# Performance work log

Measured on AMD Instinct MI355X. Metric: run time of the kernel, lower is better.

The kernel has to match this reference:

```python
import jax, jax.numpy as jnp
import numpy as np

T, H, O = 32768, 1024, 1024

def setup_inputs() -> dict:
    key = jax.random.key(0)
    k0, k1, k2 = jax.random.split(key, 3)
    dec_h = jax.random.normal(k0, (1, O), dtype=jnp.float32)
    enc = jax.random.normal(k1, (T, 1, H), dtype=jnp.float32)
    attn_w = jax.random.normal(k2, (1, O + H), dtype=jnp.float32) * 0.02
    attn_b = jnp.zeros((1,), dtype=jnp.float32)
    return {"dec_h": dec_h, "enc": enc, "attn_w": attn_w, "attn_b": attn_b}

def reference(dec_h, enc, attn_w, attn_b):
    # dec_h: [1, O]; enc: [T, 1, H]; attn_w: [1, O+H] (cat order: dec then enc)
    t, _, h = enc.shape
    o = dec_h.shape[1]
    enc2d = enc.reshape(t, h)                     # [T, H]
    w_dec = attn_w[:, :o]                         # [1, O]
    w_enc = attn_w[:, o:]                         # [1, H]
    # per-timestep Bahdanau score, vectorized over T
    scores = enc2d @ w_enc.T + (dec_h @ w_dec.T + attn_b)  # [T,1] + [1,1] -> [T,1]
    normalized_weights = jax.nn.softmax(scores.reshape(1, t), axis=1)  # [1, T]
    output = normalized_weights @ enc2d           # [1, H]
    return output, normalized_weights
```

## Files before the change

### kernel.cpp

```cpp
#include <hip/hip_runtime.h>
#include <hip/hip_bf16.h>

constexpr int T = 32768;
constexpr int H = 1024;
constexpr int NB = 512;
constexpr int RPB = T / NB;

constexpr int SC_OFF = 64;
constexpr int PART_OFF = SC_OFF + T;

__global__ void scores_kernel(const float* __restrict__ enc,
                              const float* __restrict__ w_enc,
                              float* __restrict__ scores) {
    const int gwave = (blockIdx.x * blockDim.x + threadIdx.x) >> 6;
    const int lane  = threadIdx.x & 63;
    if (gwave >= T) return;
    const float4* rowp = reinterpret_cast<const float4*>(enc + (size_t)gwave * H);
    const float4* wp   = reinterpret_cast<const float4*>(w_enc);
    float acc = 0.f;
#pragma unroll
    for (int p = 0; p < H / (64 * 4); ++p) {
        float4 e = rowp[lane + p * 64];
        float4 w = wp[lane + p * 64];
        acc += e.x * w.x + e.y * w.y + e.z * w.z + e.w * w.w;
    }
#pragma unroll
    for (int off = 32; off; off >>= 1) acc += __shfl_down(acc, off);
    if (lane == 0) scores[gwave] = acc;
}

__global__ void reduce_ml(const float* __restrict__ sc,
                          float* __restrict__ ml,
                          float* __restrict__ outvec) {
    __shared__ float sm[16];
    const int tid = threadIdx.x;
    if (tid < H) outvec[tid] = 0.f;

    float m = -1e30f;
    for (int t = tid; t < T; t += 1024) m = fmaxf(m, sc[t]);
#pragma unroll
    for (int off = 32; off; off >>= 1) m = fmaxf(m, __shfl_down(m, off));
    if ((tid & 63) == 0) sm[tid >> 6] = m;
    __syncthreads();
    if (tid < 16) {
        float v = sm[tid];
#pragma unroll
        for (int off = 8; off; off >>= 1) v = fmaxf(v, __shfl_down(v, off));
        if (tid == 0) sm[0] = v;
    }
    __syncthreads();
    const float M = sm[0];
    __syncthreads();

    float l = 0.f;
    for (int t = tid; t < T; t += 1024) l += expf(sc[t] - M);
#pragma unroll
    for (int off = 32; off; off >>= 1) l += __shfl_down(l, off);
    if ((tid & 63) == 0) sm[tid >> 6] = l;
    __syncthreads();
    if (tid == 0) {
        float L = 0.f;
#pragma unroll
        for (int i = 0; i < 16; ++i) L += sm[i];
        ml[0] = M;
        ml[1] = L;
    }
}

__global__ void weighted_kernel(const float* __restrict__ enc,
                                const float* __restrict__ sc,
                                const float* __restrict__ ml,
                                float* __restrict__ wout,
                                float* __restrict__ partials) {
    const int b = blockIdx.x;
    const int tid = threadIdx.x;
    const float M = ml[0];
    const float rL = 1.f / ml[1];
    const int row0 = b * RPB;

    if (tid < RPB) wout[row0 + tid] = expf(sc[row0 + tid] - M) * rL;

    float4 acc = make_float4(0.f, 0.f, 0.f, 0.f);
#pragma unroll 4
    for (int r = 0; r < RPB; ++r) {
        const size_t row = (size_t)(row0 + r);
        const float w = expf(sc[row] - M) * rL;
        float4 e = *reinterpret_cast<const float4*>(enc + row * H + (size_t)tid * 4);
        acc.x = fmaf(w, e.x, acc.x);
        acc.y = fmaf(w, e.y, acc.y);
        acc.z = fmaf(w, e.z, acc.z);
        acc.w = fmaf(w, e.w, acc.w);
    }
    *reinterpret_cast<float4*>(partials + (size_t)b * H + (size_t)tid * 4) = acc;
}

__global__ void finalize_kernel(const float* __restrict__ partials,
                                float* __restrict__ out) {
    const int h = blockIdx.x * blockDim.x + threadIdx.x;
    float s = 0.f;
#pragma unroll 8
    for (int b = 0; b < NB; ++b) s += partials[(size_t)b * H + h];
    out[h] = s;
}

extern "C" void kernel_launch(void* const* d_in, const int* in_sizes, int n_in,
                              void* d_out, int out_size, void* d_ws, size_t ws_size,
                              hipStream_t stream) {
    const float* enc    = (const float*)d_in[1];
    const float* attn_w = (const float*)d_in[2];
    const float* w_enc  = attn_w + 1024;

    float* out  = (float*)d_out;
    float* wout = (float*)d_out + H;

    float* ws       = (float*)d_ws;
    float* ml       = ws;
    float* scores   = ws + SC_OFF;
    float* partials = ws + PART_OFF;

    scores_kernel<<<T / 4, 256, 0, stream>>>(enc, w_enc, scores);
    reduce_ml<<<1, 1024, 0, stream>>>(scores, ml, out);
    weighted_kernel<<<NB, 256, 0, stream>>>(enc, scores, ml, wout, partials);
    finalize_kernel<<<H / 256, 256, 0, stream>>>(partials, out);
}
```

Measured before the change: 249.3 us.

## Fuse score, online softmax and weighted sum into a single pass over enc

```diff
diff --git a/kernel.cpp b/kernel.cpp
--- a/kernel.cpp
+++ b/kernel.cpp
@@ -3,104 +3,161 @@
 
 constexpr int T = 32768;
 constexpr int H = 1024;
-constexpr int NB = 512;
-constexpr int RPB = T / NB;
 
-constexpr int SC_OFF = 64;
-constexpr int PART_OFF = SC_OFF + T;
+constexpr int NB1 = 1024;
+constexpr int RPB = T / NB1;
+constexpr int CH  = 8;
 
-__global__ void scores_kernel(const float* __restrict__ enc,
-                              const float* __restrict__ w_enc,
-                              float* __restrict__ scores) {
-    const int gwave = (blockIdx.x * blockDim.x + threadIdx.x) >> 6;
-    const int lane  = threadIdx.x & 63;
-    if (gwave >= T) return;
-    const float4* rowp = reinterpret_cast<const float4*>(enc + (size_t)gwave * H);
-    const float4* wp   = reinterpret_cast<const float4*>(w_enc);
-    float acc = 0.f;
+constexpr int ML_OFF  = 0;
+constexpr int MB_OFF  = 256;
+constexpr int LB_OFF  = MB_OFF + NB1;
+constexpr int SC_OFF  = 4096;
+constexpr int ACC_OFF = SC_OFF + T;
+
+__global__ __launch_bounds__(256) void fused_pass1(
+    const float* __restrict__ enc, const float* __restrict__ w_enc,
+    float* __restrict__ scores, float* __restrict__ mb, float* __restrict__ lb,
+    float* __restrict__ accs) {
+    const int b    = blockIdx.x;
+    const int tid  = threadIdx.x;
+    const int wave = tid >> 6;
+    const int lane = tid & 63;
+    const int row0 = b * RPB;
+
+    const float4 w4 = *reinterpret_cast<const float4*>(w_enc + 4 * tid);
+
+    __shared__ float red[4][CH];
+
+    float  m = -1e30f, l = 0.f;
+    float4 acc = make_float4(0.f, 0.f, 0.f, 0.f);
+
+    for (int c = 0; c < RPB / CH; ++c) {
+        const int r0 = row0 + c * CH;
+        float4 e[CH];
+        float  p[CH];
 #pragma unroll
-    for (int p = 0; p < H / (64 * 4); ++p) {
-        float4 e = rowp[lane + p * 64];
-        float4 w = wp[lane + p * 64];
-        acc += e.x * w.x + e.y * w.y + e.z * w.z + e.w * w.w;
+        for (int r = 0; r < CH; ++r) {
+            e[r] = *reinterpret_cast<const float4*>(enc + (size_t)(r0 + r) * H + 4 * tid);
+            p[r] = e[r].x * w4.x + e[r].y * w4.y + e[r].z * w4.z + e[r].w * w4.w;
+        }
+#pragma unroll
+        for (int r = 0; r < CH; ++r) {
+#pragma unroll
+            for (int off = 32; off; off >>= 1) p[r] += __shfl_xor(p[r], off);
+        }
+        if (lane == 0) {
+#pragma unroll
+            for (int r = 0; r < CH; ++r) red[wave][r] = p[r];
+        }
+        __syncthreads();
+        float s[CH];
+        float mc = -1e30f;
+#pragma unroll
+        for (int r = 0; r < CH; ++r) {
+            s[r] = red[0][r] + red[1][r] + red[2][r] + red[3][r];
+            mc = fmaxf(mc, s[r]);
+        }
+        __syncthreads();
+
+        const float mn  = fmaxf(m, mc);
+        const float rs  = __expf(m - mn);
+        l *= rs;
+        acc.x *= rs; acc.y *= rs; acc.z *= rs; acc.w *= rs;
+#pragma unroll
+        for (int r = 0; r < CH; ++r) {
+            const float wgt = __expf(s[r] - mn);
+            l += wgt;
+            acc.x = fmaf(wgt, e[r].x, acc.x);
+            acc.y = fmaf(wgt, e[r].y, acc.y);
+            acc.z = fmaf(wgt, e[r].z, acc.z);
+            acc.w = fmaf(wgt, e[r].w, acc.w);
+        }
+        m = mn;
+
+        if (tid == 0) {
+#pragma unroll
+            for (int r = 0; r < CH; ++r) scores[r0 + r] = s[r];
+        }
     }
-#pragma unroll
-    for (int off = 32; off; off >>= 1) acc += __shfl_down(acc, off);
-    if (lane == 0) scores[gwave] = acc;
+
+    *reinterpret_cast<float4*>(accs + (size_t)b * H + 4 * tid) = acc;
+    if (tid == 0) { mb[b] = m; lb[b] = l; }
 }
 
-__global__ void reduce_ml(const float* __restrict__ sc,
-                          float* __restrict__ ml,
-                          float* __restrict__ outvec) {
+__global__ __launch_bounds__(1024) void reduce2(
+    const float* __restrict__ mb, const float* __restrict__ lb,
+    float* __restrict__ ml, float* __restrict__ out) {
     __shared__ float sm[16];
-    const int tid = threadIdx.x;
-    if (tid < H) outvec[tid] = 0.f;
+    const int tid  = threadIdx.x;
+    const int wave = tid >> 6;
+    const int lane = tid & 63;
 
-    float m = -1e30f;
-    for (int t = tid; t < T; t += 1024) m = fmaxf(m, sc[t]);
+    out[tid] = 0.f;
+
+    const float mv = mb[tid];
+    float m = mv;
 #pragma unroll
-    for (int off = 32; off; off >>= 1) m = fmaxf(m, __shfl_down(m, off));
-    if ((tid & 63) == 0) sm[tid >> 6] = m;
+    for (int off = 32; off; off >>= 1) m = fmaxf(m, __shfl_xor(m, off));
+    if (lane == 0) sm[wave] = m;
     __syncthreads();
-    if (tid < 16) {
-        float v = sm[tid];
+    if (tid < 64) {
+        float v = (lane < 16) ? sm[lane] : -1e30f;
 #pragma unroll
-        for (int off = 8; off; off >>= 1) v = fmaxf(v, __shfl_down(v, off));
+        for (int off = 8; off; off >>= 1) v = fmaxf(v, __shfl_xor(v, off));
         if (tid == 0) sm[0] = v;
     }
     __syncthreads();
     const float M = sm[0];
     __syncthreads();
 
-    float l = 0.f;
-    for (int t = tid; t < T; t += 1024) l += expf(sc[t] - M);
+    float lv = lb[tid] * __expf(mv - M);
 #pragma unroll
-    for (int off = 32; off; off >>= 1) l += __shfl_down(l, off);
-    if ((tid & 63) == 0) sm[tid >> 6] = l;
+    for (int off = 32; off; off >>= 1) lv += __shfl_xor(lv, off);
+    if (lane == 0) sm[wave] = lv;
     __syncthreads();
     if (tid == 0) {
         float L = 0.f;
 #pragma unroll
         for (int i = 0; i < 16; ++i) L += sm[i];
         ml[0] = M;
-        ml[1] = L;
+        ml[1] = 1.f / L;
     }
 }
 
-__global__ void weighted_kernel(const float* __restrict__ enc,
-                                const float* __restrict__ sc,
-                                const float* __restrict__ ml,
-                                float* __restrict__ wout,
-                                float* __restrict__ partials) {
-    const int b = blockIdx.x;
+__global__ __launch_bounds__(256) void combine3(
+    const float* __restrict__ mb, const float* __restrict__ accs,
+    const float* __restrict__ scores, const float* __restrict__ ml,
+    float* __restrict__ out, float* __restrict__ wout) {
     const int tid = threadIdx.x;
-    const float M = ml[0];
-    const float rL = 1.f / ml[1];
-    const int row0 = b * RPB;
+    const float M  = ml[0];
+    const float rL = ml[1];
 
-    if (tid < RPB) wout[row0 + tid] = expf(sc[row0 + tid] - M) * rL;
-
-    float4 acc = make_float4(0.f, 0.f, 0.f, 0.f);
+    if (blockIdx.x < 64) {
+        const int b0 = blockIdx.x * 16;
+        float4 a = make_float4(0.f, 0.f, 0.f, 0.f);
 #pragma unroll 4
-    for (int r = 0; r < RPB; ++r) {
-        const size_t row = (size_t)(row0 + r);
-        const float w = expf(sc[row] - M) * rL;
-        float4 e = *reinterpret_cast<const float4*>(enc + row * H + (size_t)tid * 4);
-        acc.x = fmaf(w, e.x, acc.x);
-        acc.y = fmaf(w, e.y, acc.y);
-        acc.z = fmaf(w, e.z, acc.z);
-        acc.w = fmaf(w, e.w, acc.w);
+        for (int i = 0; i < 16; ++i) {
+            const float wsc = __expf(mb[b0 + i] - M) * rL;
+            float4 v = *reinterpret_cast<const float4*>(accs + (size_t)(b0 + i) * H + 4 * tid);
+            a.x = fmaf(wsc, v.x, a.x);
+            a.y = fmaf(wsc, v.y, a.y);
+            a.z = fmaf(wsc, v.z, a.z);
+            a.w = fmaf(wsc, v.w, a.w);
+        }
+        atomicAdd(&out[4 * tid + 0], a.x);
+        atomicAdd(&out[4 * tid + 1], a.y);
+        atomicAdd(&out[4 * tid + 2], a.z);
+        atomicAdd(&out[4 * tid + 3], a.w);
+    } else {
+        const int t0 = (blockIdx.x - 64) * 1024 + 4 * tid;
+        float4 sv = *reinterpret_cast<const float4*>(scores + t0);
+        float4 wv;
+        wv.x = __expf(sv.x - M) * rL;
+        wv.y = __expf(sv.y - M) * rL;
+        wv.z = __expf(sv.z - M) * rL;
+        wv.w = __expf(sv.w - M) * rL;
+        *reinterpret_cast<float4*>(wout + t0) = wv;
     }
-    *reinterpret_cast<float4*>(partials + (size_t)b * H + (size_t)tid * 4) = acc;
-}
-
-__global__ void finalize_kernel(const float* __restrict__ partials,
-                                float* __restrict__ out) {
-    const int h = blockIdx.x * blockDim.x + threadIdx.x;
-    float s = 0.f;
-#pragma unroll 8
-    for (int b = 0; b < NB; ++b) s += partials[(size_t)b * H + h];
-    out[h] = s;
 }
 
 extern "C" void kernel_launch(void* const* d_in, const int* in_sizes, int n_in,
@@ -113,13 +170,14 @@
     float* out  = (float*)d_out;
     float* wout = (float*)d_out + H;
 
-    float* ws       = (float*)d_ws;
-    float* ml       = ws;
-    float* scores   = ws + SC_OFF;
-    float* partials = ws + PART_OFF;
+    float* ws     = (float*)d_ws;
+    float* ml     = ws + ML_OFF;
+    float* mb     = ws + MB_OFF;
+    float* lb     = ws + LB_OFF;
+    float* scores = ws + SC_OFF;
+    float* accs   = ws + ACC_OFF;
 
-    scores_kernel<<<T / 4, 256, 0, stream>>>(enc, w_enc, scores);
-    reduce_ml<<<1, 1024, 0, stream>>>(scores, ml, out);
-    weighted_kernel<<<NB, 256, 0, stream>>>(enc, scores, ml, wout, partials);
-    finalize_kernel<<<H / 256, 256, 0, stream>>>(partials, out);
+    fused_pass1<<<NB1, 256, 0, stream>>>(enc, w_enc, scores, mb, lb, accs);
+    reduce2<<<1, 1024, 0, stream>>>(mb, lb, ml, out);
+    combine3<<<96, 256, 0, stream>>>(mb, accs, scores, ml, out, wout);
 }
```

Result: faster. 209.9 us (-15.8%).
